# Kernel tuning notes

Measured on AMD Instinct MI355X. Metric: run time of the kernel, lower is better.

The kernel has to match this reference:

```python
import jax, jax.numpy as jnp
import numpy as np

E = 1024; H = 16; HD = E // H; T = 2048; B = 2; TOPK = E  # top_r = 1.0 -> top_k = out_features


def _dgl(x, lw, lb, g, b, w1, b1, w2, b2):
    """DGLLayer: x (l, n, c) -> (l, n, out). Top-k gated linear projection.
    Equivalent to the torch per-sample gather/matmul/scatter loop, vectorized:
    out[i, o, t] = (x @ lw.T + lb)[i, t, o] if o in topk indices of sample i else 0.
    """
    xn = jnp.transpose(x, (1, 0, 2))              # (n, l, c)
    xa = jnp.mean(xn, axis=1)                     # (n, c)  avg_pool1d over length
    mu = jnp.mean(xa, axis=-1, keepdims=True)     # LayerNorm
    var = jnp.mean((xa - mu) ** 2, axis=-1, keepdims=True)
    hn = (xa - mu) * jax.lax.rsqrt(var + 1e-5) * g + b
    logits = hn @ lw.T + lb                       # gate predictor input (linear with l_w)
    logits = jax.nn.relu(logits @ w1.T + b1)      # MLP
    logits = jax.nn.relu(logits @ w2.T + b2)
    idx = jax.lax.top_k(logits, TOPK)[1]          # (n, k)
    n = xn.shape[0]
    mask = jnp.zeros((n, lw.shape[0]), x.dtype).at[jnp.arange(n)[:, None], idx].set(1.0)
    out = (xn @ lw.T + lb) * mask[:, None, :]     # (n, l, out); zeros outside top-k
    return jnp.transpose(out, (1, 0, 2))          # (l, n, out)


def setup_inputs() -> dict:
    rng = jax.random.key(0)
    ks = jax.random.split(rng, 11)
    s = 0.02
    return {
        "query": jax.random.normal(ks[0], (T, B, E), jnp.float32),
        "key": jax.random.normal(ks[1], (T, B, E), jnp.float32),
        "value": jax.random.normal(ks[2], (T, B, E), jnp.float32),
        "in_proj_w": jax.random.normal(ks[3], (3 * E, E), jnp.float32) * s,
        "in_proj_b": jax.random.normal(ks[4], (3 * E,), jnp.float32) * s,
        "out_w": jax.random.normal(ks[5], (E, E), jnp.float32) * s,
        "out_b": jax.random.normal(ks[6], (E,), jnp.float32) * s,
        # per-DGL-layer params stacked: index 0=q, 1=k, 2=v, 3=out
        "ln_g": jnp.ones((4, E), jnp.float32),
        "ln_b": jnp.zeros((4, E), jnp.float32),
        "gw1": jax.random.normal(ks[7], (4, E, E), jnp.float32) * s,
        "gb1": jax.random.normal(ks[8], (4, E), jnp.float32) * s,
        "gw2": jax.random.normal(ks[9], (4, E, E), jnp.float32) * s,
        "gb2": jax.random.normal(ks[10], (4, E), jnp.float32) * s,
    }


def reference(query, key, value, in_proj_w, in_proj_b, out_w, out_b,
              ln_g, ln_b, gw1, gb1, gw2, gb2):
    wq, wk, wv = jnp.split(in_proj_w, 3, axis=0)
    bq, bk, bv = jnp.split(in_proj_b, 3, axis=0)
    q = _dgl(query, wq, bq, ln_g[0], ln_b[0], gw1[0], gb1[0], gw2[0], gb2[0])
    k = _dgl(key, wk, bk, ln_g[1], ln_b[1], gw1[1], gb1[1], gw2[1], gb2[1])
    v = _dgl(value, wv, bv, ln_g[2], ln_b[2], gw1[2], gb1[2], gw2[2], gb2[2])
    # (T, B, E) -> (B*H, T, HD)
    q = jnp.swapaxes(q.reshape(T, B * H, HD), 0, 1)
    k = jnp.swapaxes(k.reshape(T, B * H, HD), 0, 1)
    v = jnp.swapaxes(v.reshape(T, B * H, HD), 0, 1)
    scores = jnp.einsum('bte,bse->bts', q / np.float32(np.sqrt(HD)), k)
    attn = jax.nn.softmax(scores, axis=-1)        # (B*H, T, T)
    ao = jnp.einsum('bts,bse->bte', attn, v)
    ao = jnp.swapaxes(ao, 0, 1).reshape(T * B, E)  # (tgt*bsz, E)
    # out DGL layer sees a 2-D input -> treated as n=1, l=tgt*bsz (one global gate)
    ao = _dgl(ao[:, None, :], out_w, out_b, ln_g[3], ln_b[3], gw1[3], gb1[3], gw2[3], gb2[3])
    attn_output = ao.reshape(T, B, E)
    attn_weights = attn.reshape(B, H, T, T).mean(axis=1)  # average_attn_weights=True
    return (attn_output, attn_weights)
```

## Files before the change

### kernel.cpp

```cpp
#include <hip/hip_runtime.h>
#include <hip/hip_bf16.h>
#include <cstdint>
#include <cstddef>

#define T_DIM 2048
#define B_DIM 2
#define E_DIM 1024
#define H_DIM 16
#define HD_DIM 64
#define M_ROWS 4096
#define BH_DIM 32

typedef __attribute__((ext_vector_type(8))) short bf16x8;
typedef __attribute__((ext_vector_type(4))) float f32x4;

__device__ __forceinline__ short f2bf(float x) {
  unsigned u = __float_as_uint(x);
  u += 0x7fffu + ((u >> 16) & 1u);
  return (short)(u >> 16);
}

__device__ __forceinline__ f32x4 mfma_bf16(bf16x8 a, bf16x8 b, f32x4 c) {
  return __builtin_amdgcn_mfma_f32_16x16x32_bf16(a, b, c, 0, 0, 0);
}

__device__ __forceinline__ void gload_lds16(const void* g, void* l) {
  __builtin_amdgcn_global_load_lds(
      (const __attribute__((address_space(1))) void*)g,
      (__attribute__((address_space(3))) void*)l,
      16, 0, 0);
}

__global__ __launch_bounds__(256) void cvt_bf16_kernel(const float* __restrict__ src,
                                                       short* __restrict__ dst, int n4) {
  int i = blockIdx.x * blockDim.x + threadIdx.x;
  if (i < n4) {
    float4 v = ((const float4*)src)[i];
    short4 o;
    o.x = f2bf(v.x); o.y = f2bf(v.y); o.z = f2bf(v.z); o.w = f2bf(v.w);
    ((short4*)dst)[i] = o;
  }
}

__global__ __launch_bounds__(256) void proj_gemm_kernel(
    const short* __restrict__ A0, const short* __restrict__ W0,
    const float* __restrict__ b0,
    short* __restrict__ q_s, short* __restrict__ k_s, short* __restrict__ vT,
    float* __restrict__ outf, int mode_in) {
  int mode = (mode_in < 0) ? (int)blockIdx.z : mode_in;
  const short* A = (mode_in < 0) ? A0 + (size_t)mode * (size_t)M_ROWS * 1024 : A0;
  const short* W = W0 + (size_t)mode * 1024 * 1024;
  const float* bias = (mode_in < 0) ? b0 + mode * 1024 : b0;

  __shared__ short As[128 * 32];
  __shared__ short Bs[128 * 32];

  int tid = threadIdx.x;
  int lane = tid & 63;
  int wave = tid >> 6;
  int wm = wave >> 1, wn = wave & 1;
  int brow = blockIdx.y * 128;
  int bcol = blockIdx.x * 128;

  f32x4 acc[4][4];
#pragma unroll
  for (int i = 0; i < 4; i++)
#pragma unroll
    for (int j = 0; j < 4; j++) acc[i][j] = (f32x4){0.f, 0.f, 0.f, 0.f};

  for (int k0 = 0; k0 < 1024; k0 += 32) {
#pragma unroll
    for (int j = 0; j < 2; j++) {
      int chunk = wave * 2 + j;
      int row = chunk * 16 + (lane >> 2);
      int col = (lane & 3) * 8;
      gload_lds16(A + (size_t)(brow + row) * 1024 + k0 + col, &As[chunk * 512]);
      gload_lds16(W + (size_t)(bcol + row) * 1024 + k0 + col, &Bs[chunk * 512]);
    }
    __syncthreads();

    bf16x8 af[4], bf_[4];
#pragma unroll
    for (int mi = 0; mi < 4; mi++)
      af[mi] = *(const bf16x8*)&As[(wm * 64 + mi * 16 + (lane & 15)) * 32 + (lane >> 4) * 8];
#pragma unroll
    for (int ni = 0; ni < 4; ni++)
      bf_[ni] = *(const bf16x8*)&Bs[(wn * 64 + ni * 16 + (lane & 15)) * 32 + (lane >> 4) * 8];
#pragma unroll
    for (int mi = 0; mi < 4; mi++)
#pragma unroll
      for (int ni = 0; ni < 4; ni++)
        acc[mi][ni] = mfma_bf16(af[mi], bf_[ni], acc[mi][ni]);
    __syncthreads();
  }

#pragma unroll
  for (int mi = 0; mi < 4; mi++) {
#pragma unroll
    for (int ni = 0; ni < 4; ni++) {
      int col = bcol + wn * 64 + ni * 16 + (lane & 15);
      float bv = bias[col];
      int row0 = brow + wm * 64 + mi * 16 + (lane >> 4) * 4;
#pragma unroll
      for (int r = 0; r < 4; r++) {
        int row = row0 + r;
        float val = acc[mi][ni][r] + bv;
        int t = row >> 1, b = row & 1;
        int h = col >> 6, hd = col & 63;
        if (mode == 0) {
          q_s[((size_t)((b << 4) + h) * T_DIM + t) * HD_DIM + hd] = f2bf(val * 0.125f);
        } else if (mode == 1) {
          k_s[((size_t)((b << 4) + h) * T_DIM + t) * HD_DIM + hd] = f2bf(val);
        } else if (mode == 2) {
          vT[((size_t)((b << 4) + h) * HD_DIM + hd) * T_DIM + t] = f2bf(val);
        } else {
          outf[(size_t)row * 1024 + col] = val;
        }
      }
    }
  }
}

__device__ __forceinline__ void stage_kv(const short* kb, const short* vb, int s0,
                                         short* Ktb, short* Vtb, int tid) {
  int r0 = tid >> 3;
  int sx = (tid & 7) ^ (r0 & 7);
  gload_lds16(kb + (size_t)(s0 + r0) * 64 + sx * 8, Ktb + tid * 8);
  gload_lds16(kb + (size_t)(s0 + 32 + r0) * 64 + sx * 8, Ktb + 2048 + tid * 8);
  gload_lds16(vb + (size_t)r0 * T_DIM + s0 + sx * 8, Vtb + tid * 8);
  gload_lds16(vb + (size_t)(32 + r0) * T_DIM + s0 + sx * 8, Vtb + 2048 + tid * 8);
}

__global__ __launch_bounds__(256) void flash_fwd_kernel(
    const short* __restrict__ q_s, const short* __restrict__ k_s,
    const short* __restrict__ vT, short* __restrict__ AO,
    float* __restrict__ c_ws) {
  int bh = blockIdx.y;
  int tid = threadIdx.x;
  int lane = tid & 63;
  int wave = tid >> 6;
  int t0 = blockIdx.x * 64 + wave * 16;
  int tp = lane & 15;
  int g = lane >> 4;

  const short* qb = q_s + (size_t)bh * T_DIM * HD_DIM;
  const short* kb = k_s + (size_t)bh * T_DIM * HD_DIM;
  const short* vb = vT + (size_t)bh * HD_DIM * T_DIM;

  __shared__ short Kt[2][64 * 64];
  __shared__ short Vt[2][64 * 64];
  __shared__ short Pt[4][16 * 40];

  bf16x8 qf0 = *(const bf16x8*)&qb[(t0 + tp) * HD_DIM + g * 8];
  bf16x8 qf1 = *(const bf16x8*)&qb[(t0 + tp) * HD_DIM + 32 + g * 8];

  f32x4 acc[4];
#pragma unroll
  for (int i = 0; i < 4; i++) acc[i] = (f32x4){0.f, 0.f, 0.f, 0.f};
  float l4[4] = {0.f, 0.f, 0.f, 0.f};

  short* pl = Pt[wave];
  int sw = tp & 7;

  stage_kv(kb, vb, 0, Kt[0], Vt[0], tid);

#pragma unroll 1
  for (int i = 0; i < 32; ++i) {
    int cur = i & 1;
    __syncthreads();
    if (i + 1 < 32) stage_kv(kb, vb, (i + 1) * 64, Kt[cur ^ 1], Vt[cur ^ 1], tid);
    const short* Kc = Kt[cur];
    const short* Vc = Vt[cur];

    f32x4 S[4];
#pragma unroll
    for (int sn = 0; sn < 4; ++sn) {
      int row = sn * 16 + tp;
      bf16x8 kf0 = *(const bf16x8*)&Kc[row * 64 + (g ^ sw) * 8];
      bf16x8 kf1 = *(const bf16x8*)&Kc[row * 64 + ((g | 4) ^ sw) * 8];
      f32x4 z = (f32x4){0.f, 0.f, 0.f, 0.f};
      z = mfma_bf16(qf0, kf0, z);
      z = mfma_bf16(qf1, kf1, z);
      S[sn] = z;
    }

#pragma unroll
    for (int c32 = 0; c32 < 2; ++c32) {
#pragma unroll
      for (int snn = 0; snn < 2; ++snn) {
#pragma unroll
        for (int r = 0; r < 4; ++r) {
          float p = __expf(S[c32 * 2 + snn][r]);
          l4[r] += p;
          pl[(g * 4 + r) * 40 + snn * 16 + tp] = f2bf(p);
        }
      }
      bf16x8 pf = *(const bf16x8*)&pl[tp * 40 + g * 8];
#pragma unroll
      for (int hdt = 0; hdt < 4; ++hdt) {
        int vrow = hdt * 16 + tp;
        bf16x8 vf = *(const bf16x8*)&Vc[vrow * 64 + (((c32 * 4 + g) ^ sw)) * 8];
        acc[hdt] = mfma_bf16(pf, vf, acc[hdt]);
      }
    }
  }

  float li[4];
#pragma unroll
  for (int r = 0; r < 4; r++) {
    float v = l4[r];
    v += __shfl_xor(v, 1);
    v += __shfl_xor(v, 2);
    v += __shfl_xor(v, 4);
    v += __shfl_xor(v, 8);
    l4[r] = v;
    li[r] = 1.0f / v;
  }
  int b = bh >> 4, h = bh & 15;
#pragma unroll
  for (int hdt = 0; hdt < 4; hdt++) {
#pragma unroll
    for (int r = 0; r < 4; r++) {
      int t = t0 + g * 4 + r;
      AO[(size_t)(t * 2 + b) * E_DIM + h * 64 + hdt * 16 + tp] =
          f2bf(acc[hdt][r] * li[r]);
    }
  }
  if (tp == 0) {
#pragma unroll
    for (int r = 0; r < 4; r++) {
      int t = t0 + g * 4 + r;
      c_ws[bh * T_DIM + t] = -__logf(l4[r]);
    }
  }
}

__device__ __forceinline__ void stage_qk(const short* qh, const short* kh,
                                         int tbase, int sbase,
                                         short* Qb, short* Kb, int tid) {
  int r0 = tid >> 3;
  int sx = (tid & 7) ^ (r0 & 7);
  gload_lds16(qh + (size_t)(tbase + r0) * 64 + sx * 8, Qb + tid * 8);
  gload_lds16(qh + (size_t)(tbase + 32 + r0) * 64 + sx * 8, Qb + 2048 + tid * 8);
  gload_lds16(kh + (size_t)(sbase + r0) * 64 + sx * 8, Kb + tid * 8);
  gload_lds16(kh + (size_t)(sbase + 32 + r0) * 64 + sx * 8, Kb + 2048 + tid * 8);
}

__global__ __launch_bounds__(256) void attn_weights_kernel(
    const short* __restrict__ q_s, const short* __restrict__ k_s,
    const float* __restrict__ c_ws, float* __restrict__ wout) {
  int b = blockIdx.z;
  int tid = threadIdx.x;
  int lane = tid & 63;
  int wave = tid >> 6;
  int tbase = blockIdx.y * 64;
  int sbase = blockIdx.x * 64;
  int tp = lane & 15;
  int g = lane >> 4;
  int tw = wave * 16;
  int tq = tbase + tw + g * 4;
  int sw = tp & 7;

  __shared__ short Qt[2][64 * 64];
  __shared__ short Kt[2][64 * 64];

  float wsum[4][4];
#pragma unroll
  for (int st = 0; st < 4; st++)
#pragma unroll
    for (int r = 0; r < 4; r++) wsum[st][r] = 0.f;

  const size_t hstride = (size_t)T_DIM * HD_DIM;
  const short* qh0 = q_s + (size_t)(b * 16) * hstride;
  const short* kh0 = k_s + (size_t)(b * 16) * hstride;

  stage_qk(qh0, kh0, tbase, sbase, Qt[0], Kt[0], tid);

#pragma unroll 1
  for (int h = 0; h < 16; ++h) {
    int bh = b * 16 + h;
    int cur = h & 1;
    float4 cc = *(const float4*)&c_ws[(size_t)bh * T_DIM + tq];
    __syncthreads();
    if (h + 1 < 16)
      stage_qk(qh0 + (size_t)(h + 1) * hstride, kh0 + (size_t)(h + 1) * hstride,
               tbase, sbase, Qt[cur ^ 1], Kt[cur ^ 1], tid);
    const short* Qc = Qt[cur];
    const short* Kc = Kt[cur];

    bf16x8 qf0 = *(const bf16x8*)&Qc[(tw + tp) * 64 + (g ^ sw) * 8];
    bf16x8 qf1 = *(const bf16x8*)&Qc[(tw + tp) * 64 + ((g | 4) ^ sw) * 8];
#pragma unroll
    for (int st = 0; st < 4; ++st) {
      int row = st * 16 + tp;
      bf16x8 kf0 = *(const bf16x8*)&Kc[row * 64 + (g ^ sw) * 8];
      bf16x8 kf1 = *(const bf16x8*)&Kc[row * 64 + ((g | 4) ^ sw) * 8];
      f32x4 z = (f32x4){0.f, 0.f, 0.f, 0.f};
      z = mfma_bf16(qf0, kf0, z);
      z = mfma_bf16(qf1, kf1, z);
      wsum[st][0] += __expf(z[0] + cc.x);
      wsum[st][1] += __expf(z[1] + cc.y);
      wsum[st][2] += __expf(z[2] + cc.z);
      wsum[st][3] += __expf(z[3] + cc.w);
    }
  }

#pragma unroll
  for (int st = 0; st < 4; st++)
#pragma unroll
    for (int r = 0; r < 4; r++)
      wout[((size_t)b * T_DIM + tq + r) * T_DIM + sbase + st * 16 + tp] =
          wsum[st][r] * 0.0625f;
}

extern "C" void kernel_launch(void* const* d_in, const int* in_sizes, int n_in,
                              void* d_out, int out_size, void* d_ws, size_t ws_size,
                              hipStream_t stream) {
  const float* query = (const float*)d_in[0];
  const float* key = (const float*)d_in[1];
  const float* value = (const float*)d_in[2];
  const float* in_proj_w = (const float*)d_in[3];
  const float* in_proj_b = (const float*)d_in[4];
  const float* out_w = (const float*)d_in[5];
  const float* out_b = (const float*)d_in[6];

  float* out = (float*)d_out;
  float* wout = out + (size_t)M_ROWS * E_DIM;

  char* ws = (char*)d_ws;
  short* Wb = (short*)ws;
  short* Xb = (short*)(ws + (8ull << 20));
  short* q_s = (short*)(ws + (32ull << 20));
  short* k_s = (short*)(ws + (40ull << 20));
  short* vT = (short*)(ws + (48ull << 20));
  short* AO = (short*)(ws + (56ull << 20));
  float* c_ws = (float*)(ws + (64ull << 20));

  cvt_bf16_kernel<<<4096, 256, 0, stream>>>(query, Xb, 1048576);
  cvt_bf16_kernel<<<4096, 256, 0, stream>>>(key, Xb + 4194304, 1048576);
  cvt_bf16_kernel<<<4096, 256, 0, stream>>>(value, Xb + 8388608, 1048576);
  cvt_bf16_kernel<<<3072, 256, 0, stream>>>(in_proj_w, Wb, 786432);
  cvt_bf16_kernel<<<1024, 256, 0, stream>>>(out_w, Wb + 3145728, 262144);

  proj_gemm_kernel<<<dim3(8, 32, 3), 256, 0, stream>>>(
      Xb, Wb, in_proj_b, q_s, k_s, vT, nullptr, -1);

  flash_fwd_kernel<<<dim3(32, 32), 256, 0, stream>>>(q_s, k_s, vT, AO, c_ws);

  attn_weights_kernel<<<dim3(32, 32, 2), 256, 0, stream>>>(q_s, k_s, c_ws, wout);

  proj_gemm_kernel<<<dim3(8, 32, 1), 256, 0, stream>>>(
      AO, Wb, out_b, nullptr, nullptr, nullptr, out, 3);
}
```

Measured before the change: 205.2 us.

## Process two query tiles per wave in flash kernel and use exp2 softmax

Each wave in the flash attention kernel now handles 32 query rows as two 16-row tiles, so every K/V fragment read from LDS feeds two MFMAs, and the grid is halved. The QK product is computed transposed (K as the A operand), which lets each lane write packed bf16 P values with v_cvt_pk_bf16 and keep the row sum as a single scalar, reduced across groups at the end. Scaling by log2(e) is folded into the Q projection so both attention kernels can use the hardware exp2 instead of __expf, and the stored log-sum switches to log2. The trade-off is more registers per wave and fewer blocks to fill the device.

```diff
diff --git a/kernel.cpp b/kernel.cpp
--- a/kernel.cpp
+++ b/kernel.cpp
@@ -20,8 +20,18 @@
   return (short)(u >> 16);
 }
 
+__device__ __forceinline__ float exp2_hw(float x) {
+  return __builtin_amdgcn_exp2f(x);
+}
+
 __device__ __forceinline__ f32x4 mfma_bf16(bf16x8 a, bf16x8 b, f32x4 c) {
   return __builtin_amdgcn_mfma_f32_16x16x32_bf16(a, b, c, 0, 0, 0);
+}
+
+__device__ __forceinline__ unsigned cvt_pk_bf16(float lo, float hi) {
+  unsigned r;
+  asm volatile("v_cvt_pk_bf16_f32 %0, %1, %2" : "=v"(r) : "v"(lo), "v"(hi));
+  return r;
 }
 
 __device__ __forceinline__ void gload_lds16(const void* g, void* l) {
@@ -108,7 +118,8 @@
         int t = row >> 1, b = row & 1;
         int h = col >> 6, hd = col & 63;
         if (mode == 0) {
-          q_s[((size_t)((b << 4) + h) * T_DIM + t) * HD_DIM + hd] = f2bf(val * 0.125f);
+          q_s[((size_t)((b << 4) + h) * T_DIM + t) * HD_DIM + hd] =
+              f2bf(val * 0.1803368801f);
         } else if (mode == 1) {
           k_s[((size_t)((b << 4) + h) * T_DIM + t) * HD_DIM + hd] = f2bf(val);
         } else if (mode == 2) {
@@ -139,9 +150,10 @@
   int tid = threadIdx.x;
   int lane = tid & 63;
   int wave = tid >> 6;
-  int t0 = blockIdx.x * 64 + wave * 16;
+  int t0w = blockIdx.x * 128 + wave * 32;
   int tp = lane & 15;
   int g = lane >> 4;
+  int sw = tp & 7;
 
   const short* qb = q_s + (size_t)bh * T_DIM * HD_DIM;
   const short* kb = k_s + (size_t)bh * T_DIM * HD_DIM;
@@ -149,18 +161,23 @@
 
   __shared__ short Kt[2][64 * 64];
   __shared__ short Vt[2][64 * 64];
-  __shared__ short Pt[4][16 * 40];
-
-  bf16x8 qf0 = *(const bf16x8*)&qb[(t0 + tp) * HD_DIM + g * 8];
-  bf16x8 qf1 = *(const bf16x8*)&qb[(t0 + tp) * HD_DIM + 32 + g * 8];
-
-  f32x4 acc[4];
-#pragma unroll
-  for (int i = 0; i < 4; i++) acc[i] = (f32x4){0.f, 0.f, 0.f, 0.f};
-  float l4[4] = {0.f, 0.f, 0.f, 0.f};
-
-  short* pl = Pt[wave];
-  int sw = tp & 7;
+  __shared__ short Pt[4][2][16 * 72];
+
+  bf16x8 qfA0 = *(const bf16x8*)&qb[(t0w + tp) * HD_DIM + g * 8];
+  bf16x8 qfA1 = *(const bf16x8*)&qb[(t0w + tp) * HD_DIM + 32 + g * 8];
+  bf16x8 qfB0 = *(const bf16x8*)&qb[(t0w + 16 + tp) * HD_DIM + g * 8];
+  bf16x8 qfB1 = *(const bf16x8*)&qb[(t0w + 16 + tp) * HD_DIM + 32 + g * 8];
+
+  f32x4 accA[4], accB[4];
+#pragma unroll
+  for (int i = 0; i < 4; i++) {
+    accA[i] = (f32x4){0.f, 0.f, 0.f, 0.f};
+    accB[i] = (f32x4){0.f, 0.f, 0.f, 0.f};
+  }
+  float lA = 0.f, lB = 0.f;
+
+  short* PA = Pt[wave][0];
+  short* PB = Pt[wave][1];
 
   stage_kv(kb, vb, 0, Kt[0], Vt[0], tid);
 
@@ -172,66 +189,67 @@
     const short* Kc = Kt[cur];
     const short* Vc = Vt[cur];
 
-    f32x4 S[4];
 #pragma unroll
     for (int sn = 0; sn < 4; ++sn) {
       int row = sn * 16 + tp;
       bf16x8 kf0 = *(const bf16x8*)&Kc[row * 64 + (g ^ sw) * 8];
       bf16x8 kf1 = *(const bf16x8*)&Kc[row * 64 + ((g | 4) ^ sw) * 8];
-      f32x4 z = (f32x4){0.f, 0.f, 0.f, 0.f};
-      z = mfma_bf16(qf0, kf0, z);
-      z = mfma_bf16(qf1, kf1, z);
-      S[sn] = z;
+      f32x4 zA = (f32x4){0.f, 0.f, 0.f, 0.f};
+      zA = mfma_bf16(kf0, qfA0, zA);
+      zA = mfma_bf16(kf1, qfA1, zA);
+      f32x4 zB = (f32x4){0.f, 0.f, 0.f, 0.f};
+      zB = mfma_bf16(kf0, qfB0, zB);
+      zB = mfma_bf16(kf1, qfB1, zB);
+      float a0 = exp2_hw(zA[0]), a1 = exp2_hw(zA[1]);
+      float a2 = exp2_hw(zA[2]), a3 = exp2_hw(zA[3]);
+      float b0 = exp2_hw(zB[0]), b1 = exp2_hw(zB[1]);
+      float b2 = exp2_hw(zB[2]), b3 = exp2_hw(zB[3]);
+      lA += (a0 + a1) + (a2 + a3);
+      lB += (b0 + b1) + (b2 + b3);
+      uint2 wa, wb;
+      wa.x = cvt_pk_bf16(a0, a1); wa.y = cvt_pk_bf16(a2, a3);
+      wb.x = cvt_pk_bf16(b0, b1); wb.y = cvt_pk_bf16(b2, b3);
+      *(uint2*)&PA[tp * 72 + sn * 16 + g * 4] = wa;
+      *(uint2*)&PB[tp * 72 + sn * 16 + g * 4] = wb;
     }
 
 #pragma unroll
     for (int c32 = 0; c32 < 2; ++c32) {
-#pragma unroll
-      for (int snn = 0; snn < 2; ++snn) {
-#pragma unroll
-        for (int r = 0; r < 4; ++r) {
-          float p = __expf(S[c32 * 2 + snn][r]);
-          l4[r] += p;
-          pl[(g * 4 + r) * 40 + snn * 16 + tp] = f2bf(p);
-        }
+      bf16x8 pfA = *(const bf16x8*)&PA[tp * 72 + c32 * 32 + g * 8];
+      bf16x8 pfB = *(const bf16x8*)&PB[tp * 72 + c32 * 32 + g * 8];
+#pragma unroll
+      for (int hdt = 0; hdt < 4; ++hdt) {
+        bf16x8 vf = *(const bf16x8*)&Vc[(hdt * 16 + tp) * 64 + ((c32 * 4 + g) ^ sw) * 8];
+        accA[hdt] = mfma_bf16(pfA, vf, accA[hdt]);
+        accB[hdt] = mfma_bf16(pfB, vf, accB[hdt]);
       }
-      bf16x8 pf = *(const bf16x8*)&pl[tp * 40 + g * 8];
-#pragma unroll
-      for (int hdt = 0; hdt < 4; ++hdt) {
-        int vrow = hdt * 16 + tp;
-        bf16x8 vf = *(const bf16x8*)&Vc[vrow * 64 + (((c32 * 4 + g) ^ sw)) * 8];
-        acc[hdt] = mfma_bf16(pf, vf, acc[hdt]);
-      }
-    }
-  }
-
-  float li[4];
+    }
+  }
+
+  lA += __shfl_xor(lA, 16); lA += __shfl_xor(lA, 32);
+  lB += __shfl_xor(lB, 16); lB += __shfl_xor(lB, 32);
+  float liA[4], liB[4];
 #pragma unroll
   for (int r = 0; r < 4; r++) {
-    float v = l4[r];
-    v += __shfl_xor(v, 1);
-    v += __shfl_xor(v, 2);
-    v += __shfl_xor(v, 4);
-    v += __shfl_xor(v, 8);
-    l4[r] = v;
-    li[r] = 1.0f / v;
+    liA[r] = 1.0f / __shfl(lA, g * 4 + r);
+    liB[r] = 1.0f / __shfl(lB, g * 4 + r);
   }
   int b = bh >> 4, h = bh & 15;
 #pragma unroll
   for (int hdt = 0; hdt < 4; hdt++) {
 #pragma unroll
     for (int r = 0; r < 4; r++) {
-      int t = t0 + g * 4 + r;
-      AO[(size_t)(t * 2 + b) * E_DIM + h * 64 + hdt * 16 + tp] =
-          f2bf(acc[hdt][r] * li[r]);
-    }
-  }
-  if (tp == 0) {
-#pragma unroll
-    for (int r = 0; r < 4; r++) {
-      int t = t0 + g * 4 + r;
-      c_ws[bh * T_DIM + t] = -__logf(l4[r]);
-    }
+      int tA = t0w + g * 4 + r;
+      int tB = t0w + 16 + g * 4 + r;
+      AO[(size_t)(tA * 2 + b) * E_DIM + h * 64 + hdt * 16 + tp] =
+          f2bf(accA[hdt][r] * liA[r]);
+      AO[(size_t)(tB * 2 + b) * E_DIM + h * 64 + hdt * 16 + tp] =
+          f2bf(accB[hdt][r] * liB[r]);
+    }
+  }
+  if (lane < 16) {
+    c_ws[bh * T_DIM + t0w + tp] = -__log2f(lA);
+    c_ws[bh * T_DIM + t0w + 16 + tp] = -__log2f(lB);
   }
 }
 
@@ -298,10 +316,10 @@
       f32x4 z = (f32x4){0.f, 0.f, 0.f, 0.f};
       z = mfma_bf16(qf0, kf0, z);
       z = mfma_bf16(qf1, kf1, z);
-      wsum[st][0] += __expf(z[0] + cc.x);
-      wsum[st][1] += __expf(z[1] + cc.y);
-      wsum[st][2] += __expf(z[2] + cc.z);
-      wsum[st][3] += __expf(z[3] + cc.w);
+      wsum[st][0] += exp2_hw(z[0] + cc.x);
+      wsum[st][1] += exp2_hw(z[1] + cc.y);
+      wsum[st][2] += exp2_hw(z[2] + cc.z);
+      wsum[st][3] += exp2_hw(z[3] + cc.w);
     }
   }
 
@@ -345,7 +363,7 @@
   proj_gemm_kernel<<<dim3(8, 32, 3), 256, 0, stream>>>(
       Xb, Wb, in_proj_b, q_s, k_s, vT, nullptr, -1);
 
-  flash_fwd_kernel<<<dim3(32, 32), 256, 0, stream>>>(q_s, k_s, vT, AO, c_ws);
+  flash_fwd_kernel<<<dim3(16, 32), 256, 0, stream>>>(q_s, k_s, vT, AO, c_ws);
 
   attn_weights_kernel<<<dim3(32, 32, 2), 256, 0, stream>>>(q_s, k_s, c_ws, wout);
 
```

New measurement: 192.4 us. 1.07x faster.
